# Kernel optimization log

Hardware: AMD Instinct MI355X
Metric: run time of the kernel (lower is better)

The kernel has to match this reference:

```python
import jax, jax.numpy as jnp
import numpy as np
from jax import lax

B, N, D = 2, 2048, 1024
H = 16
DH = D // H
EXP = 4
INNER = EXP * D
KS = 3
POWER = 2
LN_EPS = 1e-5


def _layer_norm(x, g, b):
    mu = jnp.mean(x, axis=-1, keepdims=True)
    var = jnp.mean(jnp.square(x - mu), axis=-1, keepdims=True)
    return (x - mu) * lax.rsqrt(var + LN_EPS) * g + b


def setup_inputs() -> dict:
    key = jax.random.key(0)
    ks = jax.random.split(key, 12)
    s = 1.0 / np.sqrt(D)
    si = 1.0 / np.sqrt(INNER)
    return {
        "Q_in": jax.random.normal(ks[0], (B, N, D), jnp.float32),
        "X": jax.random.normal(ks[1], (B, N, D), jnp.float32),
        "Wq": jax.random.normal(ks[2], (D, D), jnp.float32) * s,
        "Wk": jax.random.normal(ks[3], (D, D), jnp.float32) * s,
        "Wv": jax.random.normal(ks[4], (D, D), jnp.float32) * s,
        "Wo": jax.random.normal(ks[5], (D, D), jnp.float32) * s,
        "Wup": jax.random.normal(ks[6], (D, 2 * INNER), jnp.float32) * s,
        "conv_w": jax.random.normal(ks[7], (INNER, 1, KS), jnp.float32) * 0.5,
        "Wdown": jax.random.normal(ks[8], (INNER, D), jnp.float32) * si,
        "g1": jnp.ones((D,), jnp.float32),
        "b1": jnp.zeros((D,), jnp.float32),
        "g2": jnp.ones((D,), jnp.float32),
        "b2": jnp.zeros((D,), jnp.float32),
        "dt": jnp.float32(0.1),
    }


def reference(Q_in, X, Wq, Wk, Wv, Wo, Wup, conv_w, Wdown, g1, b1, g2, b2, dt):
    Bn, Nn, d = Q_in.shape
    # --- attention path: kernelized quadratic attention (relu^power) ---
    Hc = _layer_norm(Q_in, g1, b1) + X                     # [B,N,d]
    def heads(x):
        return x.reshape(Bn, Nn, H, DH).transpose(0, 2, 1, 3)  # [B,H,N,dh]
    Qp = heads(Hc @ Wq)
    Kp = heads(Hc @ Wk)
    Vp = heads(Hc @ Wv)
    PhiQ = jax.nn.elu(Qp) + 1.0
    PhiK = jax.nn.elu(Kp) + 1.0
    W = jnp.einsum("bhnd,bhmd->bhnm", PhiQ, PhiK)          # [B,H,N,N]
    W = jnp.maximum(W, 0.0) ** POWER
    Attr = jnp.einsum("bhnm,bhmd->bhnd", W, Vp)
    Norm = jnp.sum(W, axis=-1, keepdims=True) + 1.0
    m = Attr / Norm - Vp                                   # [B,H,N,dh]
    m_concat = m.transpose(0, 2, 1, 3).reshape(Bn, Nn, d)
    dt_safe = jax.nn.softplus(dt)
    Q_interact = Q_in + dt_safe * (m_concat @ Wo)
    # --- gated depthwise-conv FFN (ConvSwiGLU) ---
    Qn2 = _layer_norm(Q_interact, g2, b2)
    GU = Qn2 @ Wup                                         # [B,N,2*INNER]
    G, U = GU[..., :INNER], GU[..., INNER:]
    Hf = jax.nn.silu(G) * U                                # [B,N,INNER]
    Hf_t = Hf.transpose(0, 2, 1)                           # [B,INNER,N]
    pad = (KS - 1) // 2
    Hc_t = lax.conv_general_dilated(
        Hf_t, conv_w, window_strides=(1,), padding=[(pad, pad)],
        dimension_numbers=("NCH", "OIH", "NCH"), feature_group_count=INNER)
    H_out = Hc_t.transpose(0, 2, 1) @ Wdown
    return Q_interact + H_out
```

## Files before the change

kernel.cpp:

```cpp
#include <hip/hip_runtime.h>

typedef unsigned short u16;
typedef __attribute__((ext_vector_type(8))) __bf16 bf16x8;
typedef __attribute__((ext_vector_type(4))) float f32x4;
typedef __attribute__((ext_vector_type(8))) unsigned short us8v;

__device__ __forceinline__ u16 f2bf(float x){
  union { float f; unsigned u; } v; v.f = x;
  unsigned r = v.u + 0x7fffu + ((v.u >> 16) & 1u);
  return (u16)(r >> 16);
}
__device__ __forceinline__ float bf2f(u16 h){
  union { unsigned u; float f; } v; v.u = ((unsigned)h) << 16;
  return v.f;
}
__device__ __forceinline__ void gld16(const void* g, void* l){
  __builtin_amdgcn_global_load_lds((const __attribute__((address_space(1))) unsigned int*)g,
                                   (__attribute__((address_space(3))) unsigned int*)l, 16, 0, 0);
}

__global__ __launch_bounds__(256) void tr_all(
    const float* __restrict__ Wq, const float* __restrict__ Wk,
    const float* __restrict__ Wv, const float* __restrict__ Wo,
    const float* __restrict__ Wup, const float* __restrict__ Wdown,
    u16* __restrict__ WqkvT, u16* __restrict__ WoT,
    u16* __restrict__ WupT, u16* __restrict__ WdT,
    const float* __restrict__ Qin, const float* __restrict__ X,
    const float* __restrict__ g1, const float* __restrict__ b1,
    u16* __restrict__ HcB)
{
  __shared__ float t[64][65];
  const int tid = threadIdx.x;
  const int id = blockIdx.x;
  if (id >= 4096){
    int row = id - 4096;
    const float4 x = ((const float4*)(Qin + (size_t)row*1024))[tid];
    float s = x.x + x.y + x.z + x.w;
    float sq = x.x*x.x + x.y*x.y + x.z*x.z + x.w*x.w;
    #pragma unroll
    for (int o=32;o>0;o>>=1){ s += __shfl_xor(s, o); sq += __shfl_xor(sq, o); }
    __shared__ float ss[4], ssq[4];
    int wid = tid>>6;
    if ((tid&63)==0){ ss[wid]=s; ssq[wid]=sq; }
    __syncthreads();
    s = ss[0]+ss[1]+ss[2]+ss[3]; sq = ssq[0]+ssq[1]+ssq[2]+ssq[3];
    float mu = s*(1.0f/1024.0f);
    float var = sq*(1.0f/1024.0f) - mu*mu;
    float rstd = rsqrtf(var + 1e-5f);
    float4 xx = ((const float4*)(X + (size_t)row*1024))[tid];
    float4 gv = ((const float4*)g1)[tid];
    float4 bv = ((const float4*)b1)[tid];
    ushort4 o;
    o.x = f2bf((x.x-mu)*rstd*gv.x + bv.x + xx.x);
    o.y = f2bf((x.y-mu)*rstd*gv.y + bv.y + xx.y);
    o.z = f2bf((x.z-mu)*rstd*gv.z + bv.z + xx.z);
    o.w = f2bf((x.w-mu)*rstd*gv.w + bv.w + xx.w);
    ((ushort4*)(HcB + (size_t)row*1024))[tid] = o;
    return;
  }
  const float* S; u16* D; int ldS; size_t ldD; int r0, c0; bool up = false;
  if (id < 1024){
    int w = id >> 8, b = id & 255;
    S = (w==0)?Wq:(w==1)?Wk:(w==2)?Wv:Wo;
    D = (w==3)? WoT : (WqkvT + (size_t)w*1048576);
    ldS = 1024; ldD = 1024;
    c0 = (b & 15)*64; r0 = (b >> 4)*64;
  } else if (id < 3072){
    int b = id - 1024;
    S = Wup; D = WupT; ldS = 8192; ldD = 1024; up = true;
    c0 = (b & 127)*64; r0 = (b >> 7)*64;
  } else {
    int b = id - 3072;
    S = Wdown; D = WdT; ldS = 1024; ldD = 4096;
    c0 = (b & 15)*64; r0 = (b >> 4)*64;
  }
  {
    int cr = tid >> 4, cc = (tid & 15)*4;
    #pragma unroll
    for (int j=0;j<4;j++){
      int row = cr + 16*j;
      float4 v = *(const float4*)(S + (size_t)(r0+row)*ldS + c0 + cc);
      t[row][cc+0] = v.x; t[row][cc+1] = v.y; t[row][cc+2] = v.z; t[row][cc+3] = v.w;
    }
  }
  __syncthreads();
  {
    int p = tid & 15, rg = tid >> 4;
    #pragma unroll
    for (int k=0;k<4;k++){
      int ocp = rg + 16*k;
      int oc = c0 + ocp;
      ushort4 o;
      o.x = f2bf(t[4*p+0][ocp]);
      o.y = f2bf(t[4*p+1][ocp]);
      o.z = f2bf(t[4*p+2][ocp]);
      o.w = f2bf(t[4*p+3][ocp]);
      size_t orow;
      if (up) orow = (oc < 4096) ? (size_t)((oc>>4)*32 + (oc&15))
                                 : (size_t)(((oc-4096)>>4)*32 + 16 + (oc&15));
      else    orow = (size_t)oc;
      *(ushort4*)(D + orow*ldD + r0 + 4*p) = o;
    }
  }
}

__global__ __launch_bounds__(256) void ln2_kernel(const u16* __restrict__ P,
    const float* __restrict__ Qin, const float* __restrict__ dtp,
    const float* __restrict__ g, const float* __restrict__ b,
    float* __restrict__ Qint, u16* __restrict__ Qn2){
  int row = blockIdx.x, tid = threadIdx.x;
  float sp = log1pf(__expf(dtp[0]));
  size_t off = (size_t)row*1024;
  ushort4 p0 = ((const ushort4*)(P + off))[tid];
  ushort4 p1 = ((const ushort4*)(P + 4194304 + off))[tid];
  float4 q  = ((const float4*)(Qin + off))[tid];
  float4 x;
  x.x = q.x + sp*(bf2f(p0.x)+bf2f(p1.x)); x.y = q.y + sp*(bf2f(p0.y)+bf2f(p1.y));
  x.z = q.z + sp*(bf2f(p0.z)+bf2f(p1.z)); x.w = q.w + sp*(bf2f(p0.w)+bf2f(p1.w));
  ((float4*)(Qint + off))[tid] = x;
  float s = x.x + x.y + x.z + x.w;
  float sq = x.x*x.x + x.y*x.y + x.z*x.z + x.w*x.w;
  #pragma unroll
  for (int o=32;o>0;o>>=1){ s += __shfl_xor(s, o); sq += __shfl_xor(sq, o); }
  __shared__ float ss[4], ssq[4];
  int wid = tid>>6;
  if ((tid&63)==0){ ss[wid]=s; ssq[wid]=sq; }
  __syncthreads();
  s = ss[0]+ss[1]+ss[2]+ss[3]; sq = ssq[0]+ssq[1]+ssq[2]+ssq[3];
  float mu = s*(1.0f/1024.0f);
  float var = sq*(1.0f/1024.0f) - mu*mu;
  float rstd = rsqrtf(var + 1e-5f);
  float4 gv = ((const float4*)g)[tid];
  float4 bv = ((const float4*)b)[tid];
  ushort4 o;
  o.x = f2bf((x.x-mu)*rstd*gv.x + bv.x);
  o.y = f2bf((x.y-mu)*rstd*gv.y + bv.y);
  o.z = f2bf((x.z-mu)*rstd*gv.z + bv.z);
  o.w = f2bf((x.w-mu)*rstd*gv.w + bv.w);
  ((ushort4*)(Qn2 + off))[tid] = o;
}

__global__ __launch_bounds__(256, 3) void gemm_qkv(
    const u16* __restrict__ A, const u16* __restrict__ Bt, void* __restrict__ Op)
{
  __shared__ u16 As[128*64];
  __shared__ u16 Bs[128*64];
  const int tid = threadIdx.x, wid = tid>>6, lane = tid&63;
  const int g = lane>>4, l = lane&15, l7 = l&7;
  const int row0 = blockIdx.x*128, col0 = blockIdx.y*128;
  const int wr = (wid&1)*64, wc = (wid>>1)*64;
  f32x4 acc[4][4] = {};
  for (int k0 = 0; k0 < 1024; k0 += 64){
    __syncthreads();
    #pragma unroll
    for (int i=0;i<4;i++){
      int ch0 = i*256 + wid*64;
      int ch = ch0 + lane;
      int r = ch >> 3, c = ch & 7;
      int cs = c ^ (r & 7);
      gld16(A  + (size_t)(row0+r)*1024 + k0 + cs*8, (char*)As + ch0*16);
      gld16(Bt + (size_t)(col0+r)*1024 + k0 + cs*8, (char*)Bs + ch0*16);
    }
    __syncthreads();
    #pragma unroll
    for (int kk=0; kk<2; kk++){
      bf16x8 a[4], b[4];
      #pragma unroll
      for (int i=0;i<4;i++) a[i] = *(const bf16x8*)(As + (wr + i*16 + l)*64 + (((kk*4+g)^l7)*8));
      #pragma unroll
      for (int j=0;j<4;j++) b[j] = *(const bf16x8*)(Bs + (wc + j*16 + l)*64 + (((kk*4+g)^l7)*8));
      #pragma unroll
      for (int i=0;i<4;i++)
        #pragma unroll
        for (int j=0;j<4;j++)
          acc[i][j] = __builtin_amdgcn_mfma_f32_16x16x32_bf16(a[i], b[j], acc[i][j], 0, 0, 0);
    }
  }
  u16* P = (u16*)Op;
  #pragma unroll
  for (int i=0;i<4;i++)
   #pragma unroll
   for (int j=0;j<4;j++){
     int col = col0 + wc + j*16 + l;
     int qk = col >> 10, c = col & 1023;
     int h = c >> 6, d = c & 63;
     int rowb = row0 + wr + i*16 + g*4;
     int bb = rowb >> 11, n = rowb & 2047;
     if (qk == 2){
       ushort4 vs;
       vs.x = f2bf(acc[i][j][0]); vs.y = f2bf(acc[i][j][1]);
       vs.z = f2bf(acc[i][j][2]); vs.w = f2bf(acc[i][j][3]);
       *(ushort4*)(P + (size_t)8388608 + (((size_t)(bb*16 + h))*64 + d)*2048 + n) = vs;
     } else {
       #pragma unroll
       for (int r=0;r<4;r++){
         float v = acc[i][j][r];
         float phi = v > 0.f ? v + 1.f : __expf(v);
         P[(size_t)qk*4194304 + (((size_t)(bb*16 + h))*2048 + (n+r))*64 + d] = f2bf(phi);
       }
     }
   }
}

__global__ __launch_bounds__(256, 2) void gemm_wide_up(
    const u16* __restrict__ A, const u16* __restrict__ Bt, u16* __restrict__ Op)
{
  __shared__ u16 As[256*64];
  __shared__ u16 Bs[128*64];
  const int tid = threadIdx.x, wid = tid>>6, lane = tid&63;
  const int g = lane>>4, l = lane&15, l7 = l&7;
  const int bid = blockIdx.x;
  const int bx = bid & 15;
  const int by = (bid>>7)*8 + ((bid>>4) & 7);
  const int row0 = bx*256, col0 = by*128;
  const int wr = (wid&1)*128, wc = (wid>>1)*64;
  f32x4 acc[8][4] = {};
  for (int k0 = 0; k0 < 1024; k0 += 64){
    __syncthreads();
    #pragma unroll
    for (int i=0;i<8;i++){
      int ch0 = i*256 + wid*64;
      int ch = ch0 + lane;
      int r = ch >> 3, c = ch & 7;
      int cs = c ^ (r & 7);
      gld16(A + (size_t)(row0+r)*1024 + k0 + cs*8, (char*)As + ch0*16);
    }
    #pragma unroll
    for (int i=0;i<4;i++){
      int ch0 = i*256 + wid*64;
      int ch = ch0 + lane;
      int r = ch >> 3, c = ch & 7;
      int cs = c ^ (r & 7);
      gld16(Bt + (size_t)(col0+r)*1024 + k0 + cs*8, (char*)Bs + ch0*16);
    }
    __syncthreads();
    #pragma unroll
    for (int kk=0; kk<2; kk++){
      bf16x8 a[8], b[4];
      #pragma unroll
      for (int i=0;i<8;i++) a[i] = *(const bf16x8*)(As + (wr + i*16 + l)*64 + (((kk*4+g)^l7)*8));
      #pragma unroll
      for (int j=0;j<4;j++) b[j] = *(const bf16x8*)(Bs + (wc + j*16 + l)*64 + (((kk*4+g)^l7)*8));
      #pragma unroll
      for (int i=0;i<8;i++)
        #pragma unroll
        for (int j=0;j<4;j++)
          acc[i][j] = __builtin_amdgcn_mfma_f32_16x16x32_bf16(a[i], b[j], acc[i][j], 0, 0, 0);
    }
  }
  #pragma unroll
  for (int i=0;i<8;i++)
   #pragma unroll
   for (int jj=0;jj<4;jj+=2)
    #pragma unroll
    for (int r=0;r<4;r++){
      int row = row0 + wr + i*16 + g*4 + r;
      int pair = (col0 + wc + jj*16) >> 5;
      float G = acc[i][jj][r], U = acc[i][jj+1][r];
      float hf = G/(1.f+__expf(-G))*U;
      Op[(size_t)row*4096 + pair*16 + l] = f2bf(hf);
    }
}

__global__ __launch_bounds__(256, 3) void gemm_part(
    const u16* __restrict__ A, const u16* __restrict__ Bt,
    int Nc, int K, int Ks, u16* __restrict__ Op)
{
  __shared__ u16 As[128*64];
  __shared__ u16 Bs[128*64];
  const int tid = threadIdx.x, wid = tid>>6, lane = tid&63;
  const int g = lane>>4, l = lane&15, l7 = l&7;
  const int row0 = blockIdx.x*128, col0 = blockIdx.y*128;
  const int kbase = blockIdx.z*Ks;
  const int wr = (wid&1)*64, wc = (wid>>1)*64;
  f32x4 acc[4][4] = {};
  for (int k0 = kbase; k0 < kbase + Ks; k0 += 64){
    __syncthreads();
    #pragma unroll
    for (int i=0;i<4;i++){
      int ch0 = i*256 + wid*64;
      int ch = ch0 + lane;
      int r = ch >> 3, c = ch & 7;
      int cs = c ^ (r & 7);
      gld16(A  + (size_t)(row0+r)*K + k0 + cs*8, (char*)As + ch0*16);
      gld16(Bt + (size_t)(col0+r)*K + k0 + cs*8, (char*)Bs + ch0*16);
    }
    __syncthreads();
    #pragma unroll
    for (int kk=0; kk<2; kk++){
      bf16x8 a[4], b[4];
      #pragma unroll
      for (int i=0;i<4;i++) a[i] = *(const bf16x8*)(As + (wr + i*16 + l)*64 + (((kk*4+g)^l7)*8));
      #pragma unroll
      for (int j=0;j<4;j++) b[j] = *(const bf16x8*)(Bs + (wc + j*16 + l)*64 + (((kk*4+g)^l7)*8));
      #pragma unroll
      for (int i=0;i<4;i++)
        #pragma unroll
        for (int j=0;j<4;j++)
          acc[i][j] = __builtin_amdgcn_mfma_f32_16x16x32_bf16(a[i], b[j], acc[i][j], 0, 0, 0);
    }
  }
  u16* P = Op + (size_t)blockIdx.z*4194304;
  #pragma unroll
  for (int i=0;i<4;i++)
   #pragma unroll
   for (int j=0;j<4;j++)
    #pragma unroll
    for (int r=0;r<4;r++){
      int row = row0 + wr + i*16 + g*4 + r;
      int col = col0 + wc + j*16 + l;
      P[(size_t)row*Nc + col] = f2bf(acc[i][j][r]);
    }
}

__global__ __launch_bounds__(256) void reduce_out(const float* __restrict__ Qint,
    const u16* __restrict__ P, float* __restrict__ out){
  size_t i = (size_t)blockIdx.x*256 + threadIdx.x;
  float4 a  = ((const float4*)Qint)[i];
  ushort4 p0 = ((const ushort4*)P)[i];
  ushort4 p1 = ((const ushort4*)(P + 4194304))[i];
  float4 o;
  o.x = a.x + bf2f(p0.x) + bf2f(p1.x); o.y = a.y + bf2f(p0.y) + bf2f(p1.y);
  o.z = a.z + bf2f(p0.z) + bf2f(p1.z); o.w = a.w + bf2f(p0.w) + bf2f(p1.w);
  ((float4*)out)[i] = o;
}

__global__ __launch_bounds__(256, 2) void attn_kernel(
    const u16* __restrict__ PhiQ, const u16* __restrict__ PhiK,
    const u16* __restrict__ Vt, u16* __restrict__ Mb)
{
  __shared__ u16 sK[2][128][32];
  __shared__ u16 sV[4][64][32];
  __shared__ u16 sW[128*128];
  const int tid = threadIdx.x, wid = tid>>6, lane = tid&63;
  const int g = lane>>4, l = lane&15;
  const int l3 = l & 3;
  const int q0 = blockIdx.x*128, bh = blockIdx.y;
  const u16* Q  = PhiQ + (size_t)bh*2048*64;
  const u16* Kb = PhiK + (size_t)bh*2048*64;
  const u16* V  = Vt   + (size_t)bh*64*2048;
  bf16x8 bq[8][2];
  #pragma unroll
  for (int ct=0;ct<8;ct++)
    #pragma unroll
    for (int ks=0;ks<2;ks++)
      bq[ct][ks] = *(const bf16x8*)(Q + (size_t)(q0 + ct*16 + l)*64 + ks*32 + g*8);
  f32x4 accO[2][4] = {};
  float rsum[8] = {0.f,0.f,0.f,0.f,0.f,0.f,0.f,0.f};
  for (int m0 = 0; m0 < 2048; m0 += 128){
    __syncthreads();
    #pragma unroll
    for (int ks=0; ks<2; ks++)
      #pragma unroll
      for (int i=0;i<2;i++){
        int ch0 = i*256 + wid*64;
        int ch = ch0 + lane;
        int r = ch >> 2, q = ch & 3;
        int qs = q ^ (r & 3);
        gld16(Kb + (size_t)(m0+r)*64 + ks*32 + qs*8, (char*)&sK[ks][0][0] + ch0*16);
      }
    #pragma unroll
    for (int c=0; c<4; c++){
      int ch0 = wid*64;
      int ch = ch0 + lane;
      int d = ch >> 2, q = ch & 3;
      int qs = q ^ (d & 3);
      gld16(V + (size_t)d*2048 + m0 + c*32 + qs*8, (char*)&sV[c][0][0] + ch0*16);
    }
    __syncthreads();
    f32x4 st[2][8] = {};
    bf16x8 ak[2][2];
    #pragma unroll
    for (int rt=0;rt<2;rt++)
      #pragma unroll
      for (int ks=0;ks<2;ks++)
        ak[rt][ks] = *(const bf16x8*)&sK[ks][wid*32 + rt*16 + l][(g^l3)*8];
    #pragma unroll
    for (int ct=0;ct<8;ct++){
      #pragma unroll
      for (int ks=0;ks<2;ks++){
        st[0][ct] = __builtin_amdgcn_mfma_f32_16x16x32_bf16(ak[0][ks], bq[ct][ks], st[0][ct], 0,0,0);
        st[1][ct] = __builtin_amdgcn_mfma_f32_16x16x32_bf16(ak[1][ks], bq[ct][ks], st[1][ct], 0,0,0);
      }
    }
    #pragma unroll
    for (int ct=0;ct<8;ct++){
      float part = 0.f;
      #pragma unroll
      for (int rt=0;rt<2;rt++){
        float s0 = fmaxf(st[rt][ct][0], 0.f), s1 = fmaxf(st[rt][ct][1], 0.f);
        float s2 = fmaxf(st[rt][ct][2], 0.f), s3 = fmaxf(st[rt][ct][3], 0.f);
        float w0 = s0*s0, w1 = s1*s1, w2 = s2*s2, w3 = s3*s3;
        part += w0 + w1 + w2 + w3;
        int n = ct*16 + l;
        int mblk = wid*4 + rt*2 + (g>>1);
        ushort4 w4;
        w4.x = f2bf(w0); w4.y = f2bf(w1); w4.z = f2bf(w2); w4.w = f2bf(w3);
        *(ushort4*)(sW + n*128 + ((mblk ^ l)*8) + (g&1)*4) = w4;
      }
      rsum[ct] += part;
    }
    __syncthreads();
    #pragma unroll
    for (int ks=0;ks<4;ks++){
      int n0 = wid*32 + l, n1 = wid*32 + 16 + l;
      bf16x8 aw0 = *(const bf16x8*)(sW + n0*128 + (((ks*4+g) ^ (n0&15))*8));
      bf16x8 aw1 = *(const bf16x8*)(sW + n1*128 + (((ks*4+g) ^ (n1&15))*8));
      #pragma unroll
      for (int ct=0;ct<4;ct++){
        bf16x8 bv = *(const bf16x8*)&sV[ks][ct*16 + l][(g^l3)*8];
        accO[0][ct] = __builtin_amdgcn_mfma_f32_16x16x32_bf16(aw0, bv, accO[0][ct], 0,0,0);
        accO[1][ct] = __builtin_amdgcn_mfma_f32_16x16x32_bf16(aw1, bv, accO[1][ct], 0,0,0);
      }
    }
  }
  __syncthreads();
  float* sRS = (float*)sW;
  float* sNorm = ((float*)sW) + 512;
  #pragma unroll
  for (int ct=0;ct<8;ct++){
    float v = rsum[ct];
    v += __shfl_xor(v, 16);
    v += __shfl_xor(v, 32);
    rsum[ct] = v;
  }
  if (g == 0){
    #pragma unroll
    for (int ct=0;ct<8;ct++) sRS[wid*128 + ct*16 + l] = rsum[ct];
  }
  __syncthreads();
  if (tid < 128) sNorm[tid] = sRS[tid] + sRS[128+tid] + sRS[256+tid] + sRS[384+tid] + 1.0f;
  __syncthreads();
  const int bb = bh >> 4, h = bh & 15;
  #pragma unroll
  for (int rt=0;rt<2;rt++)
   #pragma unroll
   for (int ct=0;ct<4;ct++)
    #pragma unroll
    for (int r=0;r<4;r++){
      int n = wid*32 + rt*16 + g*4 + r;
      int d = ct*16 + l;
      float norm = sNorm[n];
      float vv = bf2f(V[(size_t)d*2048 + q0 + n]);
      float mv = accO[rt][ct][r]/norm - vv;
      Mb[((size_t)(bb*2048) + q0 + n)*1024 + h*64 + d] = f2bf(mv);
    }
}

__global__ __launch_bounds__(256) void conv_kernel(const u16* __restrict__ Hf, const float* __restrict__ w,
                                                   u16* __restrict__ Cv){
  int row = blockIdx.y;
  int n = row & 2047;
  int c0 = (blockIdx.x*256 + threadIdx.x)*8;
  us8v h0 = {0,0,0,0,0,0,0,0}, h2 = {0,0,0,0,0,0,0,0};
  us8v h1 = *(const us8v*)(Hf + (size_t)row*4096 + c0);
  if (n > 0)    h0 = *(const us8v*)(Hf + (size_t)(row-1)*4096 + c0);
  if (n < 2047) h2 = *(const us8v*)(Hf + (size_t)(row+1)*4096 + c0);
  us8v o;
  #pragma unroll
  for (int e=0;e<8;e++){
    int c = c0 + e;
    float acc = bf2f(h0[e])*w[c*3+0] + bf2f(h1[e])*w[c*3+1] + bf2f(h2[e])*w[c*3+2];
    o[e] = f2bf(acc);
  }
  *(us8v*)(Cv + (size_t)row*4096 + c0) = o;
}

extern "C" void kernel_launch(void* const* d_in, const int* in_sizes, int n_in,
                              void* d_out, int out_size, void* d_ws, size_t ws_size,
                              hipStream_t stream)
{
  const float* Q_in  = (const float*)d_in[0];
  const float* X     = (const float*)d_in[1];
  const float* Wq    = (const float*)d_in[2];
  const float* Wk    = (const float*)d_in[3];
  const float* Wv    = (const float*)d_in[4];
  const float* Wo    = (const float*)d_in[5];
  const float* Wup   = (const float*)d_in[6];
  const float* convw = (const float*)d_in[7];
  const float* Wdown = (const float*)d_in[8];
  const float* g1    = (const float*)d_in[9];
  const float* b1    = (const float*)d_in[10];
  const float* g2    = (const float*)d_in[11];
  const float* b2    = (const float*)d_in[12];
  const float* dt    = (const float*)d_in[13];
  float* out = (float*)d_out;

  char* ws = (char*)d_ws;
  const size_t MB = (size_t)1 << 20;
  u16* HcB   = (u16*)(ws + 0*MB);
  u16* WqkvT = (u16*)(ws + 8*MB);
  u16* WoT   = (u16*)(ws + 14*MB);
  u16* PhiQ  = (u16*)(ws + 16*MB);
  u16* Vt    = (u16*)(ws + 32*MB);
  u16* Mb    = (u16*)(ws + 40*MB);
  u16* Po    = (u16*)(ws + 48*MB);
  u16* WupT  = (u16*)(ws + 80*MB);
  u16* WdT   = (u16*)(ws + 96*MB);
  float* Qint = (float*)(ws + 104*MB);
  u16* Qn2   = (u16*)(ws + 120*MB);
  u16* Hf    = (u16*)(ws + 0*MB);
  u16* Cv    = (u16*)(ws + 40*MB);
  u16* Pd    = (u16*)(ws + 0*MB);
  u16* PhiK  = PhiQ + 4194304;

  tr_all<<<8192, 256, 0, stream>>>(Wq, Wk, Wv, Wo, Wup, Wdown,
                                   WqkvT, WoT, WupT, WdT,
                                   Q_in, X, g1, b1, HcB);

  gemm_qkv<<<dim3(32, 24), 256, 0, stream>>>(HcB, WqkvT, PhiQ);

  attn_kernel<<<dim3(16, 32), 256, 0, stream>>>(PhiQ, PhiK, Vt, Mb);

  gemm_part<<<dim3(32, 8, 2), 256, 0, stream>>>(Mb, WoT, 1024, 1024, 512, Po);

  ln2_kernel<<<4096, 256, 0, stream>>>(Po, Q_in, dt, g2, b2, Qint, Qn2);

  gemm_wide_up<<<1024, 256, 0, stream>>>(Qn2, WupT, Hf);

  conv_kernel<<<dim3(2, 4096), 256, 0, stream>>>(Hf, convw, Cv);

  gemm_part<<<dim3(32, 8, 2), 256, 0, stream>>>(Cv, WdT, 1024, 4096, 2048, Pd);
  reduce_out<<<4096, 256, 0, stream>>>(Qint, Pd, out);
}
```

Before: 401.8 us.

## Use hardware packed bf16 conversion and a wide 4-way split-K down GEMM

```diff
diff --git a/kernel.cpp b/kernel.cpp
--- a/kernel.cpp
+++ b/kernel.cpp
@@ -13,6 +13,12 @@
 __device__ __forceinline__ float bf2f(u16 h){
   union { unsigned u; float f; } v; v.u = ((unsigned)h) << 16;
   return v.f;
+}
+__device__ __forceinline__ uint2 pkbf4(float a, float b, float c, float d){
+  uint2 r;
+  asm("v_cvt_pk_bf16_f32 %0, %1, %2" : "=v"(r.x) : "v"(a), "v"(b));
+  asm("v_cvt_pk_bf16_f32 %0, %1, %2" : "=v"(r.y) : "v"(c), "v"(d));
+  return r;
 }
 __device__ __forceinline__ void gld16(const void* g, void* l){
   __builtin_amdgcn_global_load_lds((const __attribute__((address_space(1))) unsigned int*)g,
@@ -50,12 +56,11 @@
     float4 xx = ((const float4*)(X + (size_t)row*1024))[tid];
     float4 gv = ((const float4*)g1)[tid];
     float4 bv = ((const float4*)b1)[tid];
-    ushort4 o;
-    o.x = f2bf((x.x-mu)*rstd*gv.x + bv.x + xx.x);
-    o.y = f2bf((x.y-mu)*rstd*gv.y + bv.y + xx.y);
-    o.z = f2bf((x.z-mu)*rstd*gv.z + bv.z + xx.z);
-    o.w = f2bf((x.w-mu)*rstd*gv.w + bv.w + xx.w);
-    ((ushort4*)(HcB + (size_t)row*1024))[tid] = o;
+    ((uint2*)(HcB + (size_t)row*1024))[tid] = pkbf4(
+      (x.x-mu)*rstd*gv.x + bv.x + xx.x,
+      (x.y-mu)*rstd*gv.y + bv.y + xx.y,
+      (x.z-mu)*rstd*gv.z + bv.z + xx.z,
+      (x.w-mu)*rstd*gv.w + bv.w + xx.w);
     return;
   }
   const float* S; u16* D; int ldS; size_t ldD; int r0, c0; bool up = false;
@@ -90,16 +95,12 @@
     for (int k=0;k<4;k++){
       int ocp = rg + 16*k;
       int oc = c0 + ocp;
-      ushort4 o;
-      o.x = f2bf(t[4*p+0][ocp]);
-      o.y = f2bf(t[4*p+1][ocp]);
-      o.z = f2bf(t[4*p+2][ocp]);
-      o.w = f2bf(t[4*p+3][ocp]);
+      uint2 o = pkbf4(t[4*p+0][ocp], t[4*p+1][ocp], t[4*p+2][ocp], t[4*p+3][ocp]);
       size_t orow;
       if (up) orow = (oc < 4096) ? (size_t)((oc>>4)*32 + (oc&15))
                                  : (size_t)(((oc-4096)>>4)*32 + 16 + (oc&15));
       else    orow = (size_t)oc;
-      *(ushort4*)(D + orow*ldD + r0 + 4*p) = o;
+      *(uint2*)(D + orow*ldD + r0 + 4*p) = o;
     }
   }
 }
@@ -132,12 +133,9 @@
   float rstd = rsqrtf(var + 1e-5f);
   float4 gv = ((const float4*)g)[tid];
   float4 bv = ((const float4*)b)[tid];
-  ushort4 o;
-  o.x = f2bf((x.x-mu)*rstd*gv.x + bv.x);
-  o.y = f2bf((x.y-mu)*rstd*gv.y + bv.y);
-  o.z = f2bf((x.z-mu)*rstd*gv.z + bv.z);
-  o.w = f2bf((x.w-mu)*rstd*gv.w + bv.w);
-  ((ushort4*)(Qn2 + off))[tid] = o;
+  ((uint2*)(Qn2 + off))[tid] = pkbf4(
+    (x.x-mu)*rstd*gv.x + bv.x, (x.y-mu)*rstd*gv.y + bv.y,
+    (x.z-mu)*rstd*gv.z + bv.z, (x.w-mu)*rstd*gv.w + bv.w);
 }
 
 __global__ __launch_bounds__(256, 3) void gemm_qkv(
@@ -187,10 +185,8 @@
      int rowb = row0 + wr + i*16 + g*4;
      int bb = rowb >> 11, n = rowb & 2047;
      if (qk == 2){
-       ushort4 vs;
-       vs.x = f2bf(acc[i][j][0]); vs.y = f2bf(acc[i][j][1]);
-       vs.z = f2bf(acc[i][j][2]); vs.w = f2bf(acc[i][j][3]);
-       *(ushort4*)(P + (size_t)8388608 + (((size_t)(bb*16 + h))*64 + d)*2048 + n) = vs;
+       *(uint2*)(P + (size_t)8388608 + (((size_t)(bb*16 + h))*64 + d)*2048 + n) =
+         pkbf4(acc[i][j][0], acc[i][j][1], acc[i][j][2], acc[i][j][3]);
      } else {
        #pragma unroll
        for (int r=0;r<4;r++){
@@ -262,6 +258,63 @@
     }
 }
 
+__global__ __launch_bounds__(256, 2) void gemm_wide_down(
+    const u16* __restrict__ A, const u16* __restrict__ Bt, u16* __restrict__ Op)
+{
+  __shared__ u16 As[256*64];
+  __shared__ u16 Bs[128*64];
+  const int tid = threadIdx.x, wid = tid>>6, lane = tid&63;
+  const int g = lane>>4, l = lane&15, l7 = l&7;
+  const int row0 = blockIdx.x*256, col0 = blockIdx.y*128;
+  const int kbase = blockIdx.z*1024;
+  const int wr = (wid&1)*128, wc = (wid>>1)*64;
+  f32x4 acc[8][4] = {};
+  for (int k0 = kbase; k0 < kbase + 1024; k0 += 64){
+    __syncthreads();
+    #pragma unroll
+    for (int i=0;i<8;i++){
+      int ch0 = i*256 + wid*64;
+      int ch = ch0 + lane;
+      int r = ch >> 3, c = ch & 7;
+      int cs = c ^ (r & 7);
+      gld16(A + (size_t)(row0+r)*4096 + k0 + cs*8, (char*)As + ch0*16);
+    }
+    #pragma unroll
+    for (int i=0;i<4;i++){
+      int ch0 = i*256 + wid*64;
+      int ch = ch0 + lane;
+      int r = ch >> 3, c = ch & 7;
+      int cs = c ^ (r & 7);
+      gld16(Bt + (size_t)(col0+r)*4096 + k0 + cs*8, (char*)Bs + ch0*16);
+    }
+    __syncthreads();
+    #pragma unroll
+    for (int kk=0; kk<2; kk++){
+      bf16x8 a[8], b[4];
+      #pragma unroll
+      for (int i=0;i<8;i++) a[i] = *(const bf16x8*)(As + (wr + i*16 + l)*64 + (((kk*4+g)^l7)*8));
+      #pragma unroll
+      for (int j=0;j<4;j++) b[j] = *(const bf16x8*)(Bs + (wc + j*16 + l)*64 + (((kk*4+g)^l7)*8));
+      #pragma unroll
+      for (int i=0;i<8;i++)
+        #pragma unroll
+        for (int j=0;j<4;j++)
+          acc[i][j] = __builtin_amdgcn_mfma_f32_16x16x32_bf16(a[i], b[j], acc[i][j], 0, 0, 0);
+    }
+  }
+  u16* P = Op + (size_t)blockIdx.z*4194304;
+  #pragma unroll
+  for (int i=0;i<8;i++)
+   #pragma unroll
+   for (int j=0;j<4;j++)
+    #pragma unroll
+    for (int r=0;r<4;r++){
+      int row = row0 + wr + i*16 + g*4 + r;
+      int col = col0 + wc + j*16 + l;
+      P[(size_t)row*1024 + col] = f2bf(acc[i][j][r]);
+    }
+}
+
 __global__ __launch_bounds__(256, 3) void gemm_part(
     const u16* __restrict__ A, const u16* __restrict__ Bt,
     int Nc, int K, int Ks, u16* __restrict__ Op)
@@ -319,9 +372,13 @@
   float4 a  = ((const float4*)Qint)[i];
   ushort4 p0 = ((const ushort4*)P)[i];
   ushort4 p1 = ((const ushort4*)(P + 4194304))[i];
+  ushort4 p2 = ((const ushort4*)(P + 8388608))[i];
+  ushort4 p3 = ((const ushort4*)(P + 12582912))[i];
   float4 o;
-  o.x = a.x + bf2f(p0.x) + bf2f(p1.x); o.y = a.y + bf2f(p0.y) + bf2f(p1.y);
-  o.z = a.z + bf2f(p0.z) + bf2f(p1.z); o.w = a.w + bf2f(p0.w) + bf2f(p1.w);
+  o.x = a.x + (bf2f(p0.x) + bf2f(p1.x)) + (bf2f(p2.x) + bf2f(p3.x));
+  o.y = a.y + (bf2f(p0.y) + bf2f(p1.y)) + (bf2f(p2.y) + bf2f(p3.y));
+  o.z = a.z + (bf2f(p0.z) + bf2f(p1.z)) + (bf2f(p2.z) + bf2f(p3.z));
+  o.w = a.w + (bf2f(p0.w) + bf2f(p1.w)) + (bf2f(p2.w) + bf2f(p3.w));
   ((float4*)out)[i] = o;
 }
 
@@ -391,12 +448,10 @@
         float s0 = fmaxf(st[rt][ct][0], 0.f), s1 = fmaxf(st[rt][ct][1], 0.f);
         float s2 = fmaxf(st[rt][ct][2], 0.f), s3 = fmaxf(st[rt][ct][3], 0.f);
         float w0 = s0*s0, w1 = s1*s1, w2 = s2*s2, w3 = s3*s3;
-        part += w0 + w1 + w2 + w3;
+        part += (w0 + w1) + (w2 + w3);
         int n = ct*16 + l;
         int mblk = wid*4 + rt*2 + (g>>1);
-        ushort4 w4;
-        w4.x = f2bf(w0); w4.y = f2bf(w1); w4.z = f2bf(w2); w4.w = f2bf(w3);
-        *(ushort4*)(sW + n*128 + ((mblk ^ l)*8) + (g&1)*4) = w4;
+        *(uint2*)(sW + n*128 + ((mblk ^ l)*8) + (g&1)*4) = pkbf4(w0, w1, w2, w3);
       }
       rsum[ct] += part;
     }
@@ -520,6 +575,6 @@
 
   conv_kernel<<<dim3(2, 4096), 256, 0, stream>>>(Hf, convw, Cv);
 
-  gemm_part<<<dim3(32, 8, 2), 256, 0, stream>>>(Cv, WdT, 1024, 4096, 2048, Pd);
+  gemm_wide_down<<<dim3(16, 8, 4), 256, 0, stream>>>(Cv, WdT, Pd);
   reduce_out<<<4096, 256, 0, stream>>>(Qint, Pd, out);
 }
```

Measured after the change: 382.3 us. 4.8% less time.
